# Kernel tuning notes

Hardware: AMD Instinct MI355X
Metric: run time of the kernel (lower is better)

## Reference

```python
import jax, jax.numpy as jnp
import numpy as np
import math

L, B, T, D, H, DH, DM, V = 4, 1, 2048, 1024, 16, 64, 4096, 32000
K_TOP = 512
EPS = 1e-6


def setup_inputs() -> dict:
    key = jax.random.key(0)
    ks = jax.random.split(key, 8)
    s = 0.02
    sp = 0.02 / math.sqrt(2 * L)  # c_proj special init
    return {
        "idx": jax.random.randint(ks[0], (B, T), 0, V),
        "wte": jax.random.normal(ks[1], (V, D), jnp.float32) * s,
        "wpe": jax.random.normal(ks[2], (T, D), jnp.float32) * s,
        "ln1_w": jnp.ones((L, D), jnp.float32),
        "ln2_w": jnp.ones((L, D), jnp.float32),
        "W_attn": jax.random.normal(ks[3], (L, D, 3 * H * DH), jnp.float32) * s,
        "W_attn_proj": jax.random.normal(ks[4], (L, H * DH, D), jnp.float32) * sp,
        "W_fc": jax.random.normal(ks[5], (L, D, DM), jnp.float32) * s,
        "W_mlp_proj": jax.random.normal(ks[6], (L, DM, D), jnp.float32) * sp,
        "sink_logit": jnp.zeros((L, H), jnp.float32),
        "lnf_w": jnp.ones((D,), jnp.float32),
        "lm_head_w": jax.random.normal(ks[7], (D, V), jnp.float32) * s,
        "k_topk": K_TOP,
    }


def rmsnorm(x, w):
    return x * jax.lax.rsqrt(jnp.mean(x * x, axis=-1, keepdims=True) + EPS) * w


def abs_topk(x, k):
    # zero all but the k largest-magnitude entries along the last axis
    if k >= x.shape[-1]:
        return x
    vals = jax.lax.top_k(jnp.abs(x), k)[0]
    thresh = vals[..., -1:]
    return jnp.where(jnp.abs(x) >= thresh, x, jnp.zeros((), x.dtype))


def attention_with_sink(xn, Wa, Wap, sink, causal):
    b, t, _ = xn.shape
    qkv = xn @ Wa  # [B,T,3*H*DH]
    q, k, v = jnp.split(qkv, 3, axis=-1)
    q = q.reshape(b, t, H, DH).transpose(0, 2, 1, 3)  # [B,H,T,DH]
    k = k.reshape(b, t, H, DH).transpose(0, 2, 1, 3)
    v = v.reshape(b, t, H, DH).transpose(0, 2, 1, 3)
    scale = 1.0 / math.sqrt(DH)
    scores = jnp.einsum('bhqd,bhkd->bhqk', q, k) * scale
    neg = jnp.finfo(scores.dtype).min
    scores = jnp.where(causal, scores, neg)
    # sink: zero key/value slot at position 0, logit = per-head learnable bias
    sink_col = jnp.broadcast_to(sink[None, :, None, None], (b, H, t, 1)).astype(scores.dtype)
    logits = jnp.concatenate([sink_col, scores], axis=-1)  # [B,H,T,T+1]
    probs = jax.nn.softmax(logits, axis=-1)
    y = jnp.einsum('bhqk,bhkd->bhqd', probs[..., 1:], v)  # sink v is zero
    y = y.transpose(0, 2, 1, 3).reshape(b, t, H * DH)
    return y @ Wap


def reference(idx, wte, wpe, ln1_w, ln2_w, W_attn, W_attn_proj, W_fc, W_mlp_proj,
              sink_logit, lnf_w, lm_head_w, k_topk):
    b, t = idx.shape
    x = wte[idx] + wpe[jnp.arange(t)][None]  # [B,T,D]
    causal = jnp.tril(jnp.ones((t, t), bool))

    def block(x, p):
        l1, l2, Wa, Wap, Wf, Wp, sk = p
        x = x + attention_with_sink(rmsnorm(x, l1), Wa, Wap, sk, causal)
        h = jax.nn.gelu(rmsnorm(x, l2) @ Wf, approximate=False)
        h = abs_topk(h, k_topk)  # AbsTopK at 'mlp_neuron'
        x = x + h @ Wp
        return x, None

    x, _ = jax.lax.scan(block, x, (ln1_w, ln2_w, W_attn, W_attn_proj, W_fc, W_mlp_proj, sink_logit))
    return rmsnorm(x, lnf_w) @ lm_head_w  # [B,T,V]
```

## Files before the change

### kernel.cpp

```cpp
#include <hip/hip_runtime.h>


typedef unsigned int u32;

#define TT 2048
#define DD 1024
#define HH 16
#define DMM 4096
#define VV 32000
#define AQ 4

__global__ __launch_bounds__(256) void embed32_k(const int* __restrict__ idx,
    const float* __restrict__ wte, const float* __restrict__ wpe, float* __restrict__ x){
  int t = blockIdx.x, tid = threadIdx.x;
  int tok = idx[t];
  #pragma unroll
  for (int i=0;i<4;i++){
    int e = tid*4 + i;
    x[(size_t)t*DD + e] = __fadd_rn(wte[(size_t)tok*DD + e], wpe[(size_t)t*DD + e]);
  }
}

__global__ __launch_bounds__(64) void rms_xla_k(const float* __restrict__ x,
    const float* __restrict__ w, float* __restrict__ out){
  __shared__ float sq[1024];
  __shared__ float p5[512];
  __shared__ float fin[64];
  __shared__ float srt;
  int row = blockIdx.x, lane = threadIdx.x;
  const float* xr = x + (size_t)row*DD;
  for (int i=lane; i<1024; i+=64){ float v = xr[i]; sq[i] = __fmul_rn(v,v); }
  __syncthreads();
  for (int t=lane; t<512; t+=64)
    p5[t] = __fadd_rn(sq[2*t], sq[2*t+1]);
  __syncthreads();
  #pragma unroll
  for (int off=32; off; off>>=1){
    for (int t=lane; t<8*off; t+=64){
      int wv = t/off, ii = t - wv*off;
      p5[64*wv+ii] = __fadd_rn(p5[64*wv+ii], p5[64*wv+ii+off]);
    }
    __syncthreads();
  }
  fin[lane] = (lane<8) ? p5[64*lane] : 0.0f;
  __syncthreads();
  #pragma unroll
  for (int off=32; off; off>>=1){
    if (lane<off) fin[lane] = __fadd_rn(fin[lane], fin[lane+off]);
    __syncthreads();
  }
  if (lane==0){
    float mean = __fdiv_rn(fin[0], 1024.0f);
    srt = rsqrtf(__fadd_rn(mean, 1e-6f));
  }
  __syncthreads();
  float r = srt;
  for (int i=lane; i<1024; i+=64)
    out[(size_t)row*DD + i] = __fmul_rn(__fmul_rn(xr[i], r), w[i]);
}

template<int MODE, int NQ>
__global__ __launch_bounds__(256) void gemm_db_k(const float* __restrict__ A,
    const float* __restrict__ B, float* __restrict__ C, int M, int N, int K){
  __shared__ float As[2][16][132];
  __shared__ float Bs[2][16][64*NQ+4];
  const int tid = threadIdx.x;
  const int tr = tid >> 4, tc = tid & 15;
  const int m0 = blockIdx.y*128, n0 = blockIdx.x*(64*NQ);

  const int ar0 = tid >> 2,       af0 = tid & 3;
  const int ar1 = (256+tid) >> 2, af1 = tid & 3;
  float acc[8][4*NQ];
  #pragma unroll
  for (int i=0;i<8;i++)
    #pragma unroll
    for (int j=0;j<4*NQ;j++) acc[i][j] = 0.0f;

  const int niter = K >> 4;
  {
    float4 va0 = *(const float4*)&A[(size_t)(m0+ar0)*K + 4*af0];
    float4 va1 = *(const float4*)&A[(size_t)(m0+ar1)*K + 4*af1];
    As[0][4*af0+0][ar0]=va0.x; As[0][4*af0+1][ar0]=va0.y; As[0][4*af0+2][ar0]=va0.z; As[0][4*af0+3][ar0]=va0.w;
    As[0][4*af1+0][ar1]=va1.x; As[0][4*af1+1][ar1]=va1.y; As[0][4*af1+2][ar1]=va1.z; As[0][4*af1+3][ar1]=va1.w;
    if (NQ==2){
      int r0 = tid>>5, c40 = tid&31;
      int r1 = (256+tid)>>5, c41 = tid&31;
      *(float4*)&Bs[0][r0][4*c40] = *(const float4*)&B[(size_t)r0*N + n0 + 4*c40];
      *(float4*)&Bs[0][r1][4*c41] = *(const float4*)&B[(size_t)r1*N + n0 + 4*c41];
    } else {
      int r0 = tid>>4, c40 = tid&15;
      *(float4*)&Bs[0][r0][4*c40] = *(const float4*)&B[(size_t)r0*N + n0 + 4*c40];
    }
  }
  __syncthreads();

  for (int t=0; t<niter; ++t){
    const int cur = t & 1;
    float4 va0, va1, vb0, vb1;
    if (t+1 < niter){
      int kk = (t+1) << 4;
      va0 = *(const float4*)&A[(size_t)(m0+ar0)*K + kk + 4*af0];
      va1 = *(const float4*)&A[(size_t)(m0+ar1)*K + kk + 4*af1];
      if (NQ==2){
        int r0 = tid>>5, c40 = tid&31;
        int r1 = (256+tid)>>5;
        vb0 = *(const float4*)&B[(size_t)(kk+r0)*N + n0 + 4*c40];
        vb1 = *(const float4*)&B[(size_t)(kk+r1)*N + n0 + 4*c40];
      } else {
        int r0 = tid>>4, c40 = tid&15;
        vb0 = *(const float4*)&B[(size_t)(kk+r0)*N + n0 + 4*c40];
      }
    }
    #pragma unroll 4
    for (int k=0; k<16; ++k){
      float4 a0 = *(const float4*)&As[cur][k][4*tr];
      float4 a1 = *(const float4*)&As[cur][k][64 + 4*tr];
      float4 b0 = *(const float4*)&Bs[cur][k][4*tc];
      float av[8] = {a0.x,a0.y,a0.z,a0.w, a1.x,a1.y,a1.z,a1.w};
      float bv[4*NQ];
      bv[0]=b0.x; bv[1]=b0.y; bv[2]=b0.z; bv[3]=b0.w;
      if (NQ==2){
        float4 b1 = *(const float4*)&Bs[cur][k][64 + 4*tc];
        bv[4]=b1.x; bv[5]=b1.y; bv[6]=b1.z; bv[7]=b1.w;
      }
      #pragma unroll
      for (int i=0;i<8;i++)
        #pragma unroll
        for (int j=0;j<4*NQ;j++)
          acc[i][j] = __builtin_fmaf(av[i], bv[j], acc[i][j]);
    }
    if (t+1 < niter){
      const int nxt = cur ^ 1;
      As[nxt][4*af0+0][ar0]=va0.x; As[nxt][4*af0+1][ar0]=va0.y; As[nxt][4*af0+2][ar0]=va0.z; As[nxt][4*af0+3][ar0]=va0.w;
      As[nxt][4*af1+0][ar1]=va1.x; As[nxt][4*af1+1][ar1]=va1.y; As[nxt][4*af1+2][ar1]=va1.z; As[nxt][4*af1+3][ar1]=va1.w;
      if (NQ==2){
        int r0 = tid>>5, c40 = tid&31;
        int r1 = (256+tid)>>5;
        *(float4*)&Bs[nxt][r0][4*c40] = vb0;
        *(float4*)&Bs[nxt][r1][4*c40] = vb1;
      } else {
        int r0 = tid>>4, c40 = tid&15;
        *(float4*)&Bs[nxt][r0][4*c40] = vb0;
      }
    }
    __syncthreads();
  }

  #pragma unroll
  for (int i=0;i<8;i++){
    int row = m0 + (i>>2)*64 + 4*tr + (i&3);
    #pragma unroll
    for (int jq=0;jq<NQ;jq++){
      size_t off = (size_t)row*N + n0 + jq*64 + 4*tc;
      #pragma unroll
      for (int e=0;e<4;e++){
        float vv = acc[i][jq*4+e];
        if (MODE==0){
          C[off+e] = vv;
        } else if (MODE==1){
          C[off+e] = __fadd_rn(C[off+e], vv);
        } else {
          float t2 = __fdiv_rn(vv, 1.41421356f);
          float g = erff(t2);
          C[off+e] = __fmul_rn(__fmul_rn(0.5f, vv), __fadd_rn(1.0f, g));
        }
      }
    }
  }
}

__global__ __launch_bounds__(256) void attn_v6_k(const float* __restrict__ qkv,
    const float* __restrict__ sink, float* __restrict__ y){
  __shared__ float arr[AQ][2049];
  __shared__ float Ks[64][68];
  const int tid = threadIdx.x;
  const int lane = tid & 63, wv = tid >> 6;
  const int h = blockIdx.y, q0 = blockIdx.x*AQ;
  const int qa_w = q0 + wv;
  const int qmax = q0 + AQ - 1;
  const float snk = sink[h];

  #pragma unroll
  for (int qi=0;qi<AQ;qi++)
    for (int s=tid; s<2049; s+=256) arr[qi][s] = 0.0f;

  float qv[64];
  {
    const float* qr = qkv + (size_t)qa_w*3072 + h*64;
    #pragma unroll
    for (int c4=0;c4<16;c4++){
      float4 v = *(const float4*)&qr[4*c4];
      qv[4*c4]=v.x; qv[4*c4+1]=v.y; qv[4*c4+2]=v.z; qv[4*c4+3]=v.w;
    }
  }

  float ml = -3.402823466e38f;
  for (int base=0; base<=qmax; base+=64){
    __syncthreads();
    #pragma unroll
    for (int it=0; it<4; ++it){
      int id = it*256 + tid;
      int r = id >> 4, c4 = id & 15;
      int kr = base + r;
      if (kr < TT)
        *(float4*)&Ks[r][4*c4] = *(const float4*)&qkv[(size_t)kr*3072 + 1024 + h*64 + 4*c4];
    }
    __syncthreads();
    int kv = base + lane;
    if (kv <= qa_w){
      float s = 0.0f;
      #pragma unroll
      for (int c4=0;c4<16;c4++){
        float4 kf = *(const float4*)&Ks[lane][4*c4];
        s = __builtin_fmaf(qv[4*c4  ], kf.x, s);
        s = __builtin_fmaf(qv[4*c4+1], kf.y, s);
        s = __builtin_fmaf(qv[4*c4+2], kf.z, s);
        s = __builtin_fmaf(qv[4*c4+3], kf.w, s);
      }
      s = __fmul_rn(s, 0.125f);
      arr[wv][1+kv] = s;
      ml = fmaxf(ml, s);
    }
  }
  __syncthreads();

  #pragma unroll
  for (int off=1; off<64; off<<=1) ml = fmaxf(ml, __shfl_xor(ml, off, 64));
  float m = fmaxf(ml, snk);

  for (int s=1+lane; s<=1+qa_w; s+=64)
    arr[wv][s] = expf(__fsub_rn(arr[wv][s], m));
  if (lane==0) arr[wv][0] = expf(__fsub_rn(snk, m));

  float pg[8];
  #pragma unroll
  for (int g=0; g<8; ++g){
    int t = lane + 64*g;
    float a = 0.0f;
    for (int s=t; s<2049; s+=512) a = __fadd_rn(a, arr[wv][s]);
    pg[g] = a;
  }
  #pragma unroll
  for (int g=0; g<8; ++g){
    #pragma unroll
    for (int off=32; off; off>>=1)
      pg[g] = __fadd_rn(pg[g], __shfl_down(pg[g], off, 64));
  }
  float den;
  {
    float t04 = __fadd_rn(pg[0], pg[4]);
    float t26 = __fadd_rn(pg[2], pg[6]);
    float t15 = __fadd_rn(pg[1], pg[5]);
    float t37 = __fadd_rn(pg[3], pg[7]);
    float d0 = __fadd_rn(__fadd_rn(t04, t26), __fadd_rn(t15, t37));
    den = __shfl(d0, 0, 64);
  }

  for (int s=1+lane; s<=1+qa_w; s+=64)
    arr[wv][s] = __fdiv_rn(arr[wv][s], den);

  float acc = 0.0f;
  for (int base=0; base<=qmax; base+=64){
    __syncthreads();
    #pragma unroll
    for (int it=0; it<4; ++it){
      int id = it*256 + tid;
      int r = id >> 4, c4 = id & 15;
      int kr = base + r;
      if (kr < TT)
        *(float4*)&Ks[r][4*c4] = *(const float4*)&qkv[(size_t)kr*3072 + 2048 + h*64 + 4*c4];
    }
    __syncthreads();
    int lim = qa_w - base; if (lim > 63) lim = 63;
    int j = 0;
    for (; j + 8 <= lim + 1; j += 8){
      #pragma unroll
      for (int e=0;e<8;e++)
        acc = __builtin_fmaf(arr[wv][1+base+j+e], Ks[j+e][lane], acc);
    }
    for (; j <= lim; ++j)
      acc = __builtin_fmaf(arr[wv][1+base+j], Ks[j][lane], acc);
  }
  y[(size_t)qa_w*DD + h*64 + lane] = acc;
}

__global__ __launch_bounds__(256) void topk32_k(float* __restrict__ h,
    const int* __restrict__ kptr){
  const int row = blockIdx.x, tid = threadIdx.x;
  __shared__ int suf[256];
  __shared__ int s_sel, s_k;
  float* hr = h + (size_t)row*DMM;
  int kk = kptr[0];
  u32 prefix = 0u;
  for (int pass=0; pass<4; pass++){
    int shift = 24 - 8*pass;
    u32 hi_mask = pass ? (0xFFFFFFFFu << (shift+8)) : 0u;
    suf[tid] = 0;
    __syncthreads();
    for (int i=0;i<16;i++){
      u32 b = __float_as_uint(hr[tid + 256*i]) & 0x7fffffffu;
      if ((b & hi_mask) == prefix) atomicAdd(&suf[(b>>shift)&255], 1);
    }
    __syncthreads();
    for (int s=1;s<256;s<<=1){
      int v2 = (tid+s<256) ? suf[tid+s] : 0;
      __syncthreads();
      suf[tid] += v2;
      __syncthreads();
    }
    int nxt = (tid<255) ? suf[tid+1] : 0;
    if (suf[tid] >= kk && nxt < kk){ s_sel = tid; s_k = kk - nxt; }
    __syncthreads();
    prefix |= ((u32)s_sel) << shift;
    kk = s_k;
    __syncthreads();
  }
  for (int i=0;i<16;i++){
    int e = tid + 256*i;
    u32 b = __float_as_uint(hr[e]) & 0x7fffffffu;
    if (b < prefix) hr[e] = 0.0f;
  }
}

extern "C" void kernel_launch(void* const* d_in, const int* in_sizes, int n_in,
                              void* d_out, int out_size, void* d_ws, size_t ws_size,
                              hipStream_t stream){
  const int*   idx  = (const int*)  d_in[0];
  const float* wte  = (const float*)d_in[1];
  const float* wpe  = (const float*)d_in[2];
  const float* ln1  = (const float*)d_in[3];
  const float* ln2  = (const float*)d_in[4];
  const float* Wa   = (const float*)d_in[5];
  const float* Wap  = (const float*)d_in[6];
  const float* Wf   = (const float*)d_in[7];
  const float* Wp   = (const float*)d_in[8];
  const float* sink = (const float*)d_in[9];
  const float* lnf  = (const float*)d_in[10];
  const float* lmw  = (const float*)d_in[11];
  const int*   kptr = (const int*)  d_in[12];
  (void)in_sizes; (void)n_in; (void)out_size; (void)ws_size;

  char* w = (char*)d_ws;
  float* x   = (float*)(w);
  float* xn  = (float*)(w + 8388608);
  float* qkv = (float*)(w + 16777216);
  float* y   = (float*)(w + 41943040);
  float* h   = (float*)(w + 50331648);

  embed32_k<<<TT, 256, 0, stream>>>(idx, wte, wpe, x);

  for (int l=0; l<4; l++){
    rms_xla_k<<<TT, 64, 0, stream>>>(x, ln1 + l*DD, xn);
    gemm_db_k<0,2><<<dim3(3072/128, TT/128), 256, 0, stream>>>(xn, Wa + (size_t)l*1024*3072, qkv, TT, 3072, 1024);
    attn_v6_k<<<dim3(TT/AQ, HH), 256, 0, stream>>>(qkv, sink + l*HH, y);
    gemm_db_k<1,1><<<dim3(1024/64, TT/128), 256, 0, stream>>>(y, Wap + (size_t)l*1024*1024, x, TT, 1024, 1024);
    rms_xla_k<<<TT, 64, 0, stream>>>(x, ln2 + l*DD, xn);
    gemm_db_k<2,2><<<dim3(4096/128, TT/128), 256, 0, stream>>>(xn, Wf + (size_t)l*1024*4096, h, TT, 4096, 1024);
    topk32_k<<<TT, 256, 0, stream>>>(h, kptr);
    gemm_db_k<1,1><<<dim3(1024/64, TT/128), 256, 0, stream>>>(h, Wp + (size_t)l*4096*1024, x, TT, 1024, 4096);
  }

  rms_xla_k<<<TT, 64, 0, stream>>>(x, lnf, xn);
  gemm_db_k<0,2><<<dim3(VV/128, TT/128), 256, 0, stream>>>(xn, lmw, (float*)d_out, TT, VV, 1024);
}
```

Before: 7.866 ms.

## Remap GEMM blocks XCD-aware and prefetch K/V tiles in attention

The GEMM launch becomes a 1D grid and each block index is remapped so that consecutive logical tiles, walking down M first, land on the same XCD. This groups tiles that share B columns and is meant to improve L2 reuse across MI355X's chiplets. The attention kernel now register-prefetches the next 64-row K/V chunk while the current chunk is being computed, overlapping global loads with math at the cost of extra registers. The V prefetch is issued before the softmax so its latency is hidden behind that work.

After: 10.58 ms. 34.5% more time.

```diff
diff --git a/kernel.cpp b/kernel.cpp
--- a/kernel.cpp
+++ b/kernel.cpp
@@ -61,12 +61,17 @@
 
 template<int MODE, int NQ>
 __global__ __launch_bounds__(256) void gemm_db_k(const float* __restrict__ A,
-    const float* __restrict__ B, float* __restrict__ C, int M, int N, int K){
+    const float* __restrict__ B, float* __restrict__ C, int M, int N, int K, int nm){
   __shared__ float As[2][16][132];
   __shared__ float Bs[2][16][64*NQ+4];
   const int tid = threadIdx.x;
   const int tr = tid >> 4, tc = tid & 15;
-  const int m0 = blockIdx.y*128, n0 = blockIdx.x*(64*NQ);
+  const int nwg = gridDim.x, w0 = blockIdx.x;
+  const int qq = nwg >> 3, rr8 = nwg & 7;
+  const int xcd = w0 & 7, jj = w0 >> 3;
+  const int lid = xcd*qq + (xcd < rr8 ? xcd : rr8) + jj;
+  const int bm = lid % nm, bn = lid / nm;
+  const int m0 = bm*128, n0 = bn*(64*NQ);
 
   const int ar0 = tid >> 2,       af0 = tid & 3;
   const int ar1 = (256+tid) >> 2, af1 = tid & 3;
@@ -169,7 +174,7 @@
   }
 }
 
-__global__ __launch_bounds__(256) void attn_v6_k(const float* __restrict__ qkv,
+__global__ __launch_bounds__(256) void attn_v7_k(const float* __restrict__ qkv,
     const float* __restrict__ sink, float* __restrict__ y){
   __shared__ float arr[AQ][2049];
   __shared__ float Ks[64][68];
@@ -178,7 +183,9 @@
   const int h = blockIdx.y, q0 = blockIdx.x*AQ;
   const int qa_w = q0 + wv;
   const int qmax = q0 + AQ - 1;
+  const int nch = (qmax >> 6) + 1;
   const float snk = sink[h];
+  const int sr = tid >> 4, sc4 = tid & 15;
 
   #pragma unroll
   for (int qi=0;qi<AQ;qi++)
@@ -195,17 +202,25 @@
   }
 
   float ml = -3.402823466e38f;
-  for (int base=0; base<=qmax; base+=64){
-    __syncthreads();
-    #pragma unroll
-    for (int it=0; it<4; ++it){
-      int id = it*256 + tid;
-      int r = id >> 4, c4 = id & 15;
-      int kr = base + r;
-      if (kr < TT)
-        *(float4*)&Ks[r][4*c4] = *(const float4*)&qkv[(size_t)kr*3072 + 1024 + h*64 + 4*c4];
-    }
-    __syncthreads();
+  float4 ld[4];
+  #pragma unroll
+  for (int it=0; it<4; ++it)
+    ld[it] = *(const float4*)&qkv[(size_t)(sr + it*16)*3072 + 1024 + h*64 + 4*sc4];
+  for (int c=0; c<nch; ++c){
+    int base = c << 6;
+    #pragma unroll
+    for (int it=0; it<4; ++it)
+      *(float4*)&Ks[sr + it*16][4*sc4] = ld[it];
+    __syncthreads();
+    if (c+1 < nch){
+      int nb = base + 64;
+      #pragma unroll
+      for (int it=0; it<4; ++it){
+        int kr = nb + sr + it*16;
+        if (kr < TT)
+          ld[it] = *(const float4*)&qkv[(size_t)kr*3072 + 1024 + h*64 + 4*sc4];
+      }
+    }
     int kv = base + lane;
     if (kv <= qa_w){
       float s = 0.0f;
@@ -221,8 +236,12 @@
       arr[wv][1+kv] = s;
       ml = fmaxf(ml, s);
     }
-  }
-  __syncthreads();
+    __syncthreads();
+  }
+
+  #pragma unroll
+  for (int it=0; it<4; ++it)
+    ld[it] = *(const float4*)&qkv[(size_t)(sr + it*16)*3072 + 2048 + h*64 + 4*sc4];
 
   #pragma unroll
   for (int off=1; off<64; off<<=1) ml = fmaxf(ml, __shfl_xor(ml, off, 64));
@@ -260,17 +279,22 @@
     arr[wv][s] = __fdiv_rn(arr[wv][s], den);
 
   float acc = 0.0f;
-  for (int base=0; base<=qmax; base+=64){
-    __syncthreads();
-    #pragma unroll
-    for (int it=0; it<4; ++it){
-      int id = it*256 + tid;
-      int r = id >> 4, c4 = id & 15;
-      int kr = base + r;
-      if (kr < TT)
-        *(float4*)&Ks[r][4*c4] = *(const float4*)&qkv[(size_t)kr*3072 + 2048 + h*64 + 4*c4];
-    }
-    __syncthreads();
+  for (int c=0; c<nch; ++c){
+    int base = c << 6;
+    __syncthreads();
+    #pragma unroll
+    for (int it=0; it<4; ++it)
+      *(float4*)&Ks[sr + it*16][4*sc4] = ld[it];
+    __syncthreads();
+    if (c+1 < nch){
+      int nb = base + 64;
+      #pragma unroll
+      for (int it=0; it<4; ++it){
+        int kr = nb + sr + it*16;
+        if (kr < TT)
+          ld[it] = *(const float4*)&qkv[(size_t)kr*3072 + 2048 + h*64 + 4*sc4];
+      }
+    }
     int lim = qa_w - base; if (lim > 63) lim = 63;
     int j = 0;
     for (; j + 8 <= lim + 1; j += 8){
@@ -351,15 +375,15 @@
 
   for (int l=0; l<4; l++){
     rms_xla_k<<<TT, 64, 0, stream>>>(x, ln1 + l*DD, xn);
-    gemm_db_k<0,2><<<dim3(3072/128, TT/128), 256, 0, stream>>>(xn, Wa + (size_t)l*1024*3072, qkv, TT, 3072, 1024);
-    attn_v6_k<<<dim3(TT/AQ, HH), 256, 0, stream>>>(qkv, sink + l*HH, y);
-    gemm_db_k<1,1><<<dim3(1024/64, TT/128), 256, 0, stream>>>(y, Wap + (size_t)l*1024*1024, x, TT, 1024, 1024);
+    gemm_db_k<0,2><<<(3072/128)*(TT/128), 256, 0, stream>>>(xn, Wa + (size_t)l*1024*3072, qkv, TT, 3072, 1024, TT/128);
+    attn_v7_k<<<dim3(TT/AQ, HH), 256, 0, stream>>>(qkv, sink + l*HH, y);
+    gemm_db_k<1,1><<<(1024/64)*(TT/128), 256, 0, stream>>>(y, Wap + (size_t)l*1024*1024, x, TT, 1024, 1024, TT/128);
     rms_xla_k<<<TT, 64, 0, stream>>>(x, ln2 + l*DD, xn);
-    gemm_db_k<2,2><<<dim3(4096/128, TT/128), 256, 0, stream>>>(xn, Wf + (size_t)l*1024*4096, h, TT, 4096, 1024);
+    gemm_db_k<2,2><<<(4096/128)*(TT/128), 256, 0, stream>>>(xn, Wf + (size_t)l*1024*4096, h, TT, 4096, 1024, TT/128);
     topk32_k<<<TT, 256, 0, stream>>>(h, kptr);
-    gemm_db_k<1,1><<<dim3(1024/64, TT/128), 256, 0, stream>>>(h, Wp + (size_t)l*4096*1024, x, TT, 1024, 4096);
+    gemm_db_k<1,1><<<(1024/64)*(TT/128), 256, 0, stream>>>(h, Wp + (size_t)l*4096*1024, x, TT, 1024, 4096, TT/128);
   }
 
   rms_xla_k<<<TT, 64, 0, stream>>>(x, lnf, xn);
-  gemm_db_k<0,2><<<dim3(VV/128, TT/128), 256, 0, stream>>>(xn, lmw, (float*)d_out, TT, VV, 1024);
-}
+  gemm_db_k<0,2><<<(VV/128)*(TT/128), 256, 0, stream>>>(xn, lmw, (float*)d_out, TT, VV, 1024, TT/128);
+}
```
